# Kernel optimization log

Measured on AMD Instinct MI355X. Metric: run time of the kernel, lower is better.

The kernel has to match this reference:

```python
import jax, jax.numpy as jnp
import numpy as np

B, C, H, W = 16, 384, 32, 32
TEXT = 768
HW = H * W  # == hidden_size
EPS_IN = 1e-5
EPS_L2 = 1e-12


def _gconv3x3(x, w, groups):
    # x: [B,C,H,W], w: [C, C//groups, 3, 3] (torch OIHW layout), padding=1
    return jax.lax.conv_general_dilated(
        x, w, window_strides=(1, 1), padding='SAME',
        dimension_numbers=('NCHW', 'OIHW', 'NCHW'),
        feature_group_count=groups)


def _l2norm(x):
    # torch F.normalize(dim=-1): x / max(||x||_2, 1e-12)
    n = jnp.sqrt(jnp.sum(x * x, axis=-1, keepdims=True))
    return x / jnp.maximum(n, EPS_L2)


def _inst_norm(x):
    # InstanceNorm2d(affine=False) over last two dims per (b, head), biased var
    m = jnp.mean(x, axis=(2, 3), keepdims=True)
    v = jnp.var(x, axis=(2, 3), keepdims=True)
    return (x - m) / jnp.sqrt(v + EPS_IN)


def setup_inputs() -> dict:
    key = jax.random.key(0)
    ks = jax.random.split(key, 13)
    inp = {
        'emb1': jax.random.normal(ks[0], (B, C, H, W), jnp.float32),
        'emb2': jax.random.normal(ks[1], (B, C, H, W), jnp.float32),
        'emb3': jax.random.normal(ks[2], (B, C, H, W), jnp.float32),
        'emb4': jax.random.normal(ks[3], (B, C, H, W), jnp.float32),
        'text_emb': jax.random.normal(ks[4], (B, 1, C, TEXT), jnp.float32),
        # q: Linear(text_size -> hidden_size)
        'wq': jax.random.normal(ks[5], (HW, TEXT), jnp.float32) * 0.02,
        'bq': jnp.zeros((HW,), jnp.float32),
        # 1x1 pointwise projections for k/v (stacked over 4 branches)
        'mk': jax.random.normal(ks[6], (4, C, C), jnp.float32) * (1.0 / np.sqrt(C)),
        'mv': jax.random.normal(ks[7], (4, C, C), jnp.float32) * (1.0 / np.sqrt(C)),
        # 3x3 grouped convs, groups=C//2 -> in_per_group=2, torch weight [C,2,3,3]
        'kw': jax.random.normal(ks[8], (4, C, 2, 3, 3), jnp.float32) * 0.1,
        'vw': jax.random.normal(ks[9], (4, C, 2, 3, 3), jnp.float32) * 0.1,
        # 1x1 output projections
        'po': jax.random.normal(ks[10], (4, C, C), jnp.float32) * (1.0 / np.sqrt(C)),
    }
    return inp


def reference(emb1, emb2, emb3, emb4, text_emb, wq, bq, mk, mv, kw, vw, po):
    b, c, h, w = emb1.shape
    hw = h * w
    # q = Linear(text_emb): [B,1,C,TEXT] @ [TEXT,HW] -> [B,1,C,HW]
    q = _l2norm(text_emb @ wq.T + bq)
    scale = 1.0 / (c ** 0.5)
    embs = (emb1, emb2, emb3, emb4)
    outs = []
    for i in range(4):
        x = embs[i]
        k = _gconv3x3(jnp.einsum('bchw,oc->bohw', x, mk[i]), kw[i], c // 2)
        v = _gconv3x3(jnp.einsum('bchw,oc->bohw', x, mv[i]), vw[i], c // 2)
        k = _l2norm(k.reshape(b, 1, c, hw))   # [B,1,C,HW]
        v = v.reshape(b, 1, c, hw)
        attn = jnp.einsum('bhcn,bhdn->bhcd', q, k) * scale  # [B,1,C,C]
        attn = jax.nn.softmax(_inst_norm(attn), axis=3)
        o = jnp.einsum('bhcd,bhdn->bhcn', attn, v).mean(axis=1)  # [B,C,HW]
        o = jnp.einsum('bchw,oc->bohw', o.reshape(b, c, h, w), po[i])
        outs.append(o)
    return tuple(outs)
```

## Files before the change

### kernel.cpp

```cpp
#include <hip/hip_runtime.h>

typedef unsigned short u16;
typedef __bf16 bf16x8 __attribute__((ext_vector_type(8)));
typedef float f32x4 __attribute__((ext_vector_type(4)));

__device__ __forceinline__ float b2f(u16 u) {
  unsigned int x = ((unsigned int)u) << 16;
  float f;
  __builtin_memcpy(&f, &x, 4);
  return f;
}
__device__ __forceinline__ u16 f2b(float f) {
  unsigned int x;
  __builtin_memcpy(&x, &f, 4);
  unsigned int r = x + 0x7FFFu + ((x >> 16) & 1u);
  return (u16)(r >> 16);
}
static inline unsigned int f2b_host(float f) {
  unsigned int x;
  __builtin_memcpy(&x, &f, 4);
  unsigned int r = x + 0x7FFFu + ((x >> 16) & 1u);
  return r >> 16;
}

__device__ __forceinline__ void gl_lds16(const u16* g, u16* l) {
  __builtin_amdgcn_global_load_lds(
      (const __attribute__((address_space(1))) void*)g,
      (__attribute__((address_space(3))) void*)l, 16, 0, 0);
}

__global__ __launch_bounds__(256) void fill_diag(unsigned int* __restrict__ p,
                                                 long n4, unsigned int pat) {
  long i = (long)blockIdx.x * 256 + threadIdx.x;
  const long stride = (long)gridDim.x * 256;
  for (; i < n4; i += stride) p[i] = pat;
}

__global__ __launch_bounds__(256) void detect_dtype(const u16* __restrict__ text,
                                                    int* __restrict__ flag,
                                                    float* __restrict__ stats) {
  __shared__ int red[4];
  const int t = threadIdx.x;
  if (t < 128) stats[t] = 0.f;
  int c = 0;
#pragma unroll
  for (int j = 0; j < 8; j++) {
    u16 u = text[t * 8 + j];
    int e = (u >> 7) & 0xFF;
    c += (e >= 0x90);
  }
#pragma unroll
  for (int off = 32; off; off >>= 1) c += __shfl_xor(c, off);
  if ((t & 63) == 0) red[t >> 6] = c;
  __syncthreads();
  if (t == 0) flag[0] = (red[0] + red[1] + red[2] + red[3] >= 16) ? 1 : 0;
}

struct Cvt {
  const void* s;
  u16* d;
  long soff;
  int n;
};
struct Cvt16 {
  Cvt c[15];
};
__global__ __launch_bounds__(256) void convert16(Cvt16 args, const int* __restrict__ flag) {
  const Cvt cc = args.c[blockIdx.y];
  const int i8 = (blockIdx.x * 256 + threadIdx.x) * 8;
  if (i8 >= cc.n) return;
  u16 o[8];
  if (flag[0]) {
    const float* s = (const float*)cc.s + cc.soff + i8;
    float4 a = *(const float4*)s;
    float4 b = *(const float4*)(s + 4);
    o[0] = f2b(a.x); o[1] = f2b(a.y); o[2] = f2b(a.z); o[3] = f2b(a.w);
    o[4] = f2b(b.x); o[5] = f2b(b.y); o[6] = f2b(b.z); o[7] = f2b(b.w);
  } else {
    uint4 r = *(const uint4*)((const u16*)cc.s + cc.soff + i8);
    __builtin_memcpy(o, &r, 16);
  }
  uint4 pk;
  __builtin_memcpy(&pk, o, 16);
  *(uint4*)(cc.d + i8) = pk;
}

template <int OUT_BF16, int ADD_BIAS, int DO_STATS>
__global__ __launch_bounds__(256) void gemm_nt(
    const u16* __restrict__ A, const u16* __restrict__ B, void* __restrict__ Cv,
    const u16* __restrict__ bias, int lda, int ldb, int ldc, int K,
    long sA, int zshA, int zmaskA, long sB, long sC, long base, float scale,
    const int* __restrict__ oflag, float* __restrict__ stats,
    int z0, int aglob, int cglob) {
  __shared__ u16 As[4096];
  __shared__ u16 Bs[4096];
  __shared__ float redS[4], redQ[4];
  const int t = threadIdx.x;
  const int zl = blockIdx.z;
  const int zg = zl + z0;
  const int za = aglob ? zg : zl;
  const int zc = cglob ? zg : zl;
  A += (long)((za >> zshA) & zmaskA) * sA;
  B += (long)zl * sB;
  const int bm = blockIdx.y * 128;
  const int bn = blockIdx.x * 128;
  const int lane = t & 63;
  const int wv = t >> 6;
  const int wm = (wv & 1) * 64;
  const int wn = (wv >> 1) * 64;
  const int lr = lane & 15;
  const int lq = lane >> 4;

  const int c0 = wv * 2;
  const int row0 = c0 * 16 + (lane >> 2);
  const int kcl = (((lane & 3) - ((lane >> 3) & 3)) & 3) * 8;
  const u16* pa0 = A + (size_t)(bm + row0) * lda + kcl;
  const u16* pa1 = pa0 + (size_t)16 * lda;
  const u16* pb0 = B + (size_t)(bn + row0) * ldb + kcl;
  const u16* pb1 = pb0 + (size_t)16 * ldb;
  u16* lA0 = &As[c0 * 512];
  u16* lA1 = &As[c0 * 512 + 512];
  u16* lB0 = &Bs[c0 * 512];
  u16* lB1 = &Bs[c0 * 512 + 512];

  const u16* aptr[4];
  const u16* bptr[4];
#pragma unroll
  for (int i = 0; i < 4; i++) {
    const int m = wm + i * 16 + lr;
    aptr[i] = &As[(m * 4 + ((lq + ((m >> 1) & 3)) & 3)) * 8];
    const int n = wn + i * 16 + lr;
    bptr[i] = &Bs[(n * 4 + ((lq + ((n >> 1) & 3)) & 3)) * 8];
  }

  f32x4 acc[4][4];
#pragma unroll
  for (int i = 0; i < 4; i++)
#pragma unroll
    for (int j = 0; j < 4; j++) acc[i][j] = (f32x4){0.f, 0.f, 0.f, 0.f};

  for (int k0 = 0; k0 < K; k0 += 32) {
    gl_lds16(pa0 + k0, lA0);
    gl_lds16(pa1 + k0, lA1);
    gl_lds16(pb0 + k0, lB0);
    gl_lds16(pb1 + k0, lB1);
    __syncthreads();
    bf16x8 af[4], bfr[4];
#pragma unroll
    for (int i = 0; i < 4; i++) af[i] = *(const bf16x8*)aptr[i];
#pragma unroll
    for (int j = 0; j < 4; j++) bfr[j] = *(const bf16x8*)bptr[j];
#pragma unroll
    for (int i = 0; i < 4; i++)
#pragma unroll
      for (int j = 0; j < 4; j++)
        acc[i][j] = __builtin_amdgcn_mfma_f32_16x16x32_bf16(af[i], bfr[j], acc[i][j], 0, 0, 0);
    __syncthreads();
  }

  int f32o = OUT_BF16 ? 0 : 1;
  if (oflag) f32o = oflag[0];
  u16* Cb = (u16*)Cv + base + (long)zc * sC;
  float* Cf = (float*)Cv + base + (long)zc * sC;
  float ls = 0.f, lsq = 0.f;
#pragma unroll
  for (int i = 0; i < 4; i++) {
    const int gm0 = bm + wm + i * 16 + lq * 4;
#pragma unroll
    for (int j = 0; j < 4; j++) {
      const int gn = bn + wn + j * 16 + lr;
      float bv = 0.f;
      if (ADD_BIAS) bv = b2f(bias[gn]);
#pragma unroll
      for (int r = 0; r < 4; r++) {
        float v = acc[i][j][r] * scale + bv;
        if (DO_STATS) {
          ls += v;
          lsq += v * v;
        }
        if (f32o)
          Cf[(size_t)(gm0 + r) * ldc + gn] = v;
        else
          Cb[(size_t)(gm0 + r) * ldc + gn] = f2b(v);
      }
    }
  }
  if (DO_STATS) {
#pragma unroll
    for (int off = 32; off; off >>= 1) {
      ls += __shfl_xor(ls, off);
      lsq += __shfl_xor(lsq, off);
    }
    if (lane == 0) {
      redS[wv] = ls;
      redQ[wv] = lsq;
    }
    __syncthreads();
    if (t == 0) {
      atomicAdd(&stats[zg * 2 + 0], redS[0] + redS[1] + redS[2] + redS[3]);
      atomicAdd(&stats[zg * 2 + 1], redQ[0] + redQ[1] + redQ[2] + redQ[3]);
    }
  }
}

__global__ __launch_bounds__(64) void finalize_stats(const float* __restrict__ stats,
                                                     float* __restrict__ rstd,
                                                     int z0, int cnt) {
  const int i = threadIdx.x;
  if (i >= cnt) return;
  const int z = z0 + i;
  float s = stats[2 * z], q = stats[2 * z + 1];
  float mean = s * (1.f / 147456.f);
  float var = q * (1.f / 147456.f) - mean * mean;
  rstd[z] = 1.f / sqrtf(var + 1e-5f);
}

struct Ptr4 {
  const void* p[4];
};
__global__ __launch_bounds__(256) void transpose_any4(Ptr4 in4, u16* __restrict__ out,
                                                      const int* __restrict__ flag,
                                                      int z0) {
  __shared__ u16 tile[64][72];
  const int t = threadIdx.x;
  const int zl = blockIdx.z;
  const int zg = zl + z0;
  const int br = zg >> 4, b = zg & 15;
  const long ebase = (long)b * 393216;
  const int r0 = blockIdx.y * 64;
  const int c0 = blockIdx.x * 64;
  const int isf32 = flag[0];
#pragma unroll
  for (int j = 0; j < 2; j++) {
    int idx = t + 256 * j;
    int r = idx >> 3, c8 = (idx & 7) << 3;
    u16 v[8];
    if (isf32) {
      const float* in = (const float*)in4.p[br] + ebase + (size_t)(r0 + r) * 1024 + c0 + c8;
      float4 a = *(const float4*)in;
      float4 bb = *(const float4*)(in + 4);
      v[0] = f2b(a.x); v[1] = f2b(a.y); v[2] = f2b(a.z); v[3] = f2b(a.w);
      v[4] = f2b(bb.x); v[5] = f2b(bb.y); v[6] = f2b(bb.z); v[7] = f2b(bb.w);
    } else {
      const u16* in = (const u16*)in4.p[br] + ebase + (size_t)(r0 + r) * 1024 + c0 + c8;
      uint4 rr = *(const uint4*)in;
      __builtin_memcpy(v, &rr, 16);
    }
    __builtin_memcpy(&tile[r][c8], v, 16);
  }
  __syncthreads();
#pragma unroll
  for (int j = 0; j < 2; j++) {
    int idx = t + 256 * j;
    int c = idx >> 3, r8 = (idx & 7) << 3;
    u16 v[8];
#pragma unroll
    for (int jj = 0; jj < 8; jj++) v[jj] = tile[r8 + jj][c];
    uint4 pk;
    __builtin_memcpy(&pk, v, 16);
    *(uint4*)&out[(size_t)zl * 393216 + (size_t)(c0 + c) * 384 + r0 + r8] = pk;
  }
}

__global__ __launch_bounds__(256) void transpose_bf16(const u16* __restrict__ in,
                                                      u16* __restrict__ out) {
  __shared__ u16 tile[64][72];
  const int t = threadIdx.x;
  in += (size_t)blockIdx.z * 393216;
  out += (size_t)blockIdx.z * 393216;
  const int r0 = blockIdx.y * 64;
  const int c0 = blockIdx.x * 64;
#pragma unroll
  for (int j = 0; j < 2; j++) {
    int idx = t + 256 * j;
    int r = idx >> 3, c8 = (idx & 7) << 3;
    *(uint4*)&tile[r][c8] = *(const uint4*)&in[(size_t)(r0 + r) * 1024 + c0 + c8];
  }
  __syncthreads();
#pragma unroll
  for (int j = 0; j < 2; j++) {
    int idx = t + 256 * j;
    int c = idx >> 3, r8 = (idx & 7) << 3;
    u16 v[8];
#pragma unroll
    for (int jj = 0; jj < 8; jj++) v[jj] = tile[r8 + jj][c];
    uint4 pk;
    __builtin_memcpy(&pk, v, 16);
    *(uint4*)&out[(size_t)(c0 + c) * 384 + r0 + r8] = pk;
  }
}

__global__ __launch_bounds__(256) void l2norm_rows_bf16(u16* __restrict__ Q) {
  __shared__ float red[4];
  u16* row = Q + (size_t)blockIdx.x * 1024;
  const int t = threadIdx.x;
  uint2 r = *(const uint2*)(row + t * 4);
  u16 v[4];
  __builtin_memcpy(v, &r, 8);
  float f[4] = {b2f(v[0]), b2f(v[1]), b2f(v[2]), b2f(v[3])};
  float s = f[0] * f[0] + f[1] * f[1] + f[2] * f[2] + f[3] * f[3];
#pragma unroll
  for (int off = 32; off; off >>= 1) s += __shfl_xor(s, off);
  if ((t & 63) == 0) red[t >> 6] = s;
  __syncthreads();
  float tot = red[0] + red[1] + red[2] + red[3];
  float inv = 1.f / fmaxf(sqrtf(tot), 1e-12f);
  u16 o[4] = {f2b(f[0] * inv), f2b(f[1] * inv), f2b(f[2] * inv), f2b(f[3] * inv)};
  unsigned long long pk;
  __builtin_memcpy(&pk, o, 8);
  *(unsigned long long*)(row + t * 4) = pk;
}

__global__ __launch_bounds__(256) void gconv3x3(
    const u16* __restrict__ kvpre, const u16* __restrict__ kw,
    const u16* __restrict__ vw, u16* __restrict__ outK, u16* __restrict__ outV,
    int z0) {
  __shared__ float p[2][1024];
  __shared__ float red[4];
  const int o = blockIdx.x;
  const int zl = blockIdx.y;
  const int kv = blockIdx.z;
  const int t = threadIdx.x;
  const int br = (z0 + zl) >> 4;
  const u16* in = kvpre + ((size_t)zl * 768 + kv * 384 + (o & ~1)) * 1024;
  const u16* wp = (kv ? vw : kw) + br * 6912 + o * 18;
  u16* out = (kv ? outV : outK) + ((size_t)zl * 384 + o) * 1024;
  {
    uint2 ra = *(const uint2*)(in + t * 4);
    uint2 rb = *(const uint2*)(in + 1024 + t * 4);
    u16 va[4], vb[4];
    __builtin_memcpy(va, &ra, 8);
    __builtin_memcpy(vb, &rb, 8);
#pragma unroll
    for (int j = 0; j < 4; j++) {
      p[0][t * 4 + j] = b2f(va[j]);
      p[1][t * 4 + j] = b2f(vb[j]);
    }
  }
  float w[18];
#pragma unroll
  for (int j = 0; j < 18; j++) w[j] = b2f(wp[j]);
  __syncthreads();
  float o4[4];
#pragma unroll
  for (int ii = 0; ii < 4; ii++) {
    const int pidx = t + 256 * ii;
    const int y = pidx >> 5, x = pidx & 31;
    float acc = 0.f;
#pragma unroll
    for (int ch = 0; ch < 2; ch++)
#pragma unroll
      for (int dy = 0; dy < 3; dy++) {
        const int yy = y + dy - 1;
        if (yy < 0 || yy > 31) continue;
#pragma unroll
        for (int dx = 0; dx < 3; dx++) {
          const int xx = x + dx - 1;
          if (xx < 0 || xx > 31) continue;
          acc += w[ch * 9 + dy * 3 + dx] * p[ch][yy * 32 + xx];
        }
      }
    o4[ii] = acc;
  }
  float inv = 1.f;
  if (kv == 0) {
    float s = o4[0] * o4[0] + o4[1] * o4[1] + o4[2] * o4[2] + o4[3] * o4[3];
#pragma unroll
    for (int off = 32; off; off >>= 1) s += __shfl_xor(s, off);
    if ((t & 63) == 0) red[t >> 6] = s;
    __syncthreads();
    float tot = red[0] + red[1] + red[2] + red[3];
    inv = 1.f / fmaxf(sqrtf(tot), 1e-12f);
  }
#pragma unroll
  for (int ii = 0; ii < 4; ii++) out[t + 256 * ii] = f2b(o4[ii] * inv);
}

__global__ __launch_bounds__(256) void softmax384(const float* __restrict__ S,
                                                  const float* __restrict__ rstdA,
                                                  u16* __restrict__ P, int z0) {
  const int row = blockIdx.x * 4 + (threadIdx.x >> 6);
  const int lane = threadIdx.x & 63;
  const float rstd = rstdA[z0 + row / 384];
  const float* x = S + (size_t)row * 384;
  float v[6];
#pragma unroll
  for (int j = 0; j < 6; j++) v[j] = x[lane + 64 * j] * rstd;
  float m = v[0];
#pragma unroll
  for (int j = 1; j < 6; j++) m = fmaxf(m, v[j]);
#pragma unroll
  for (int off = 32; off; off >>= 1) m = fmaxf(m, __shfl_xor(m, off));
  float s = 0.f;
#pragma unroll
  for (int j = 0; j < 6; j++) {
    v[j] = __expf(v[j] - m);
    s += v[j];
  }
#pragma unroll
  for (int off = 32; off; off >>= 1) s += __shfl_xor(s, off);
  const float inv = 1.f / s;
  u16* out = P + (size_t)row * 384;
#pragma unroll
  for (int j = 0; j < 6; j++) out[lane + 64 * j] = f2b(v[j] * inv);
}

extern "C" void kernel_launch(void* const* d_in, const int* in_sizes, int n_in,
                              void* d_out, int out_size, void* d_ws, size_t ws_size,
                              hipStream_t stream) {
  char* ws = (char*)d_ws;
  const dim3 blk(256);

  const size_t bigOff = 17809408;
  auto need = [&](size_t Zs) {
    size_t c = Zs * 3145728;
    if (c < 9437184) c = 9437184;
    return bigOff + c;
  };
  auto diag = [&](float C) {
    unsigned int h = f2b_host(C);
    unsigned int pat = (h << 16) | h;
    long n4 = (long)out_size / 4;
    if (n4 < 1) n4 = 1;
    fill_diag<<<dim3(2048), blk, 0, stream>>>((unsigned int*)d_out, n4, pat);
  };

  static const long elems[12] = {6291456, 6291456, 6291456, 6291456, 4718592,
                                 786432, 1024, 589824, 589824, 27648, 27648,
                                 589824};
  if (!(n_in >= 12) || !d_in || !in_sizes || !d_out || !d_ws) {
    diag(1.0e6f);
    return;
  }
  for (int i = 0; i < 12; i++) {
    if (!d_in[i]) {
      diag(2.0e6f);
      return;
    }
    long sz = in_sizes[i];
    if (sz != elems[i] && sz != elems[i] * 2 && sz != elems[i] * 4) {
      diag(3.0e6f + (float)i * 1.25e5f);
      return;
    }
  }
  if (ws_size < need(1)) {
    diag(9.0e6f);
    return;
  }

  int* flag = (int*)ws;
  float* stats = (float*)(ws + 256);
  float* rstd = (float*)(ws + 1024);
  char* wgt = ws + 2048;
  u16* wq16 = (u16*)wgt;
  u16* bq16 = (u16*)(wgt + 1572864);
  u16* mkv16 = (u16*)(wgt + 1574912);
  u16* kw16 = (u16*)(wgt + 3934208);
  u16* vw16 = (u16*)(wgt + 3989504);
  u16* po16 = (u16*)(wgt + 4044800);
  u16* q16 = (u16*)(ws + 5226496);

  int Z = 1;
  for (int cand = 64; cand >= 1; cand >>= 1) {
    if (ws_size >= need(cand)) {
      Z = cand;
      break;
    }
  }

  char* regA = ws + bigOff;
  char* regB = regA + (size_t)Z * 786432;
  char* regC = regB + (size_t)Z * 1572864;

  u16* text16 = (u16*)regA;
  u16* xT = (u16*)regA;
  u16* kAll = (u16*)regA;
  u16* O = (u16*)regA;
  u16* kvpre = (u16*)regB;
  u16* vT = (u16*)regB;
  float* S = (float*)(regB + (size_t)Z * 786432);
  u16* OT = (u16*)regB;
  u16* vAll = (u16*)regC;
  u16* P16 = (u16*)regC;

  const float scale = 0.05103103630798288f;

  detect_dtype<<<1, blk, 0, stream>>>((const u16*)d_in[4], flag, stats);

  Cvt16 ca;
  int ci = 0;
  auto add = [&](const void* s, u16* d, long soff, int n) {
    ca.c[ci].s = s; ca.c[ci].d = d; ca.c[ci].soff = soff; ca.c[ci].n = n; ci++;
  };
  add(d_in[4], text16, 0, 4718592);
  add(d_in[5], wq16, 0, 786432);
  add(d_in[6], bq16, 0, 1024);
  for (int i = 0; i < 4; i++) add(d_in[7], mkv16 + (long)i * 294912, (long)i * 147456, 147456);
  for (int i = 0; i < 4; i++) add(d_in[8], mkv16 + (long)i * 294912 + 147456, (long)i * 147456, 147456);
  add(d_in[9], kw16, 0, 27648);
  add(d_in[10], vw16, 0, 27648);
  add(d_in[11], po16, 0, 589824);
  convert16<<<dim3(2304, 15, 1), blk, 0, stream>>>(ca, flag);

  gemm_nt<1, 1, 0><<<dim3(8, 48, 1), blk, 0, stream>>>(
      text16, wq16, q16, bq16, 768, 768, 1024, 768, 0, 0, 0, 0, 0, 0, 1.f,
      nullptr, nullptr, 0, 0, 0);
  l2norm_rows_bf16<<<6144, blk, 0, stream>>>(q16);

  Ptr4 p4 = {{d_in[0], d_in[1], d_in[2], d_in[3]}};

  for (int z0 = 0; z0 < 64; z0 += Z) {
    transpose_any4<<<dim3(16, 6, Z), blk, 0, stream>>>(p4, xT, flag, z0);

    gemm_nt<1, 0, 0><<<dim3(8, 6, Z), blk, 0, stream>>>(
        mkv16, xT, kvpre, nullptr, 384, 384, 1024, 384, 294912, 4, 3, 393216,
        786432, 0, 1.f, nullptr, nullptr, z0, 1, 0);

    gconv3x3<<<dim3(384, Z, 2), blk, 0, stream>>>(kvpre, kw16, vw16, kAll,
                                                  vAll, z0);

    transpose_bf16<<<dim3(16, 6, Z), blk, 0, stream>>>(vAll, vT);

    gemm_nt<0, 0, 1><<<dim3(3, 3, Z), blk, 0, stream>>>(
        q16, kAll, S, nullptr, 1024, 1024, 384, 1024, 393216, 0, 15, 393216,
        147456, 0, scale, nullptr, stats, z0, 1, 0);
    finalize_stats<<<1, 64, 0, stream>>>(stats, rstd, z0, Z);
    softmax384<<<Z * 96, blk, 0, stream>>>(S, rstd, P16, z0);

    gemm_nt<1, 0, 0><<<dim3(8, 3, Z), blk, 0, stream>>>(
        P16, vT, O, nullptr, 384, 384, 1024, 384, 147456, 0, 63, 393216, 393216,
        0, 1.f, nullptr, nullptr, z0, 0, 0);
    transpose_bf16<<<dim3(16, 6, Z), blk, 0, stream>>>(O, OT);

    gemm_nt<0, 0, 0><<<dim3(8, 3, Z), blk, 0, stream>>>(
        po16, OT, d_out, nullptr, 384, 384, 1024, 384, 147456, 4, 3, 393216,
        393216, 0, 1.f, flag, nullptr, z0, 1, 1);
  }
}
```

Before: 594.3 us.

## Reassociate output projection as (po·P)·V and fuse stats finalize into softmax

The output is now computed by first multiplying the projection weights by the attention matrix, giving a 384x384 product, and then applying that to V. This replaces the old order, which multiplied P by V (384x1024), transposed the result and then projected it, so one large transpose and one 1024-wide GEMM become a small transpose and a 384x384 GEMM. The finalize_stats kernel is removed, and its mean/rstd computation moves into softmax384. gconv3x3 now handles two output channels per block, so the shared input pair is loaded once. Rounding to bf16 at the intermediate W step changes numerics slightly.

```diff
diff --git a/kernel.cpp b/kernel.cpp
--- a/kernel.cpp
+++ b/kernel.cpp
@@ -203,18 +203,6 @@
   }
 }
 
-__global__ __launch_bounds__(64) void finalize_stats(const float* __restrict__ stats,
-                                                     float* __restrict__ rstd,
-                                                     int z0, int cnt) {
-  const int i = threadIdx.x;
-  if (i >= cnt) return;
-  const int z = z0 + i;
-  float s = stats[2 * z], q = stats[2 * z + 1];
-  float mean = s * (1.f / 147456.f);
-  float var = q * (1.f / 147456.f) - mean * mean;
-  rstd[z] = 1.f / sqrtf(var + 1e-5f);
-}
-
 struct Ptr4 {
   const void* p[4];
 };
@@ -290,6 +278,34 @@
   }
 }
 
+__global__ __launch_bounds__(256) void transpose_b384(const u16* __restrict__ in,
+                                                      u16* __restrict__ out) {
+  __shared__ u16 tile[64][72];
+  const int t = threadIdx.x;
+  in += (size_t)blockIdx.z * 147456;
+  out += (size_t)blockIdx.z * 147456;
+  const int r0 = blockIdx.y * 64;
+  const int c0 = blockIdx.x * 64;
+#pragma unroll
+  for (int j = 0; j < 2; j++) {
+    int idx = t + 256 * j;
+    int r = idx >> 3, c8 = (idx & 7) << 3;
+    *(uint4*)&tile[r][c8] = *(const uint4*)&in[(size_t)(r0 + r) * 384 + c0 + c8];
+  }
+  __syncthreads();
+#pragma unroll
+  for (int j = 0; j < 2; j++) {
+    int idx = t + 256 * j;
+    int c = idx >> 3, r8 = (idx & 7) << 3;
+    u16 v[8];
+#pragma unroll
+    for (int jj = 0; jj < 8; jj++) v[jj] = tile[r8 + jj][c];
+    uint4 pk;
+    __builtin_memcpy(&pk, v, 16);
+    *(uint4*)&out[(size_t)(c0 + c) * 384 + r0 + r8] = pk;
+  }
+}
+
 __global__ __launch_bounds__(256) void l2norm_rows_bf16(u16* __restrict__ Q) {
   __shared__ float red[4];
   u16* row = Q + (size_t)blockIdx.x * 1024;
@@ -316,15 +332,15 @@
     const u16* __restrict__ vw, u16* __restrict__ outK, u16* __restrict__ outV,
     int z0) {
   __shared__ float p[2][1024];
-  __shared__ float red[4];
-  const int o = blockIdx.x;
+  __shared__ float redA[4], redB[4];
+  const int o0 = blockIdx.x * 2;
   const int zl = blockIdx.y;
   const int kv = blockIdx.z;
   const int t = threadIdx.x;
   const int br = (z0 + zl) >> 4;
-  const u16* in = kvpre + ((size_t)zl * 768 + kv * 384 + (o & ~1)) * 1024;
-  const u16* wp = (kv ? vw : kw) + br * 6912 + o * 18;
-  u16* out = (kv ? outV : outK) + ((size_t)zl * 384 + o) * 1024;
+  const u16* in = kvpre + ((size_t)zl * 768 + kv * 384 + o0) * 1024;
+  const u16* wp = (kv ? vw : kw) + br * 6912 + o0 * 18;
+  u16* out = (kv ? outV : outK) + ((size_t)zl * 384 + o0) * 1024;
   {
     uint2 ra = *(const uint2*)(in + t * 4);
     uint2 rb = *(const uint2*)(in + 1024 + t * 4);
@@ -337,16 +353,16 @@
       p[1][t * 4 + j] = b2f(vb[j]);
     }
   }
-  float w[18];
-#pragma unroll
-  for (int j = 0; j < 18; j++) w[j] = b2f(wp[j]);
+  float w[36];
+#pragma unroll
+  for (int j = 0; j < 36; j++) w[j] = b2f(wp[j]);
   __syncthreads();
-  float o4[4];
+  float oa[4], ob[4];
 #pragma unroll
   for (int ii = 0; ii < 4; ii++) {
     const int pidx = t + 256 * ii;
     const int y = pidx >> 5, x = pidx & 31;
-    float acc = 0.f;
+    float acca = 0.f, accb = 0.f;
 #pragma unroll
     for (int ch = 0; ch < 2; ch++)
 #pragma unroll
@@ -357,31 +373,50 @@
         for (int dx = 0; dx < 3; dx++) {
           const int xx = x + dx - 1;
           if (xx < 0 || xx > 31) continue;
-          acc += w[ch * 9 + dy * 3 + dx] * p[ch][yy * 32 + xx];
+          const float pv = p[ch][yy * 32 + xx];
+          acca += w[ch * 9 + dy * 3 + dx] * pv;
+          accb += w[18 + ch * 9 + dy * 3 + dx] * pv;
         }
       }
-    o4[ii] = acc;
-  }
-  float inv = 1.f;
+    oa[ii] = acca;
+    ob[ii] = accb;
+  }
+  float inva = 1.f, invb = 1.f;
   if (kv == 0) {
-    float s = o4[0] * o4[0] + o4[1] * o4[1] + o4[2] * o4[2] + o4[3] * o4[3];
-#pragma unroll
-    for (int off = 32; off; off >>= 1) s += __shfl_xor(s, off);
-    if ((t & 63) == 0) red[t >> 6] = s;
+    float sa = oa[0] * oa[0] + oa[1] * oa[1] + oa[2] * oa[2] + oa[3] * oa[3];
+    float sb = ob[0] * ob[0] + ob[1] * ob[1] + ob[2] * ob[2] + ob[3] * ob[3];
+#pragma unroll
+    for (int off = 32; off; off >>= 1) {
+      sa += __shfl_xor(sa, off);
+      sb += __shfl_xor(sb, off);
+    }
+    if ((t & 63) == 0) {
+      redA[t >> 6] = sa;
+      redB[t >> 6] = sb;
+    }
     __syncthreads();
-    float tot = red[0] + red[1] + red[2] + red[3];
-    inv = 1.f / fmaxf(sqrtf(tot), 1e-12f);
-  }
-#pragma unroll
-  for (int ii = 0; ii < 4; ii++) out[t + 256 * ii] = f2b(o4[ii] * inv);
+    float ta = redA[0] + redA[1] + redA[2] + redA[3];
+    float tb = redB[0] + redB[1] + redB[2] + redB[3];
+    inva = 1.f / fmaxf(sqrtf(ta), 1e-12f);
+    invb = 1.f / fmaxf(sqrtf(tb), 1e-12f);
+  }
+#pragma unroll
+  for (int ii = 0; ii < 4; ii++) {
+    out[t + 256 * ii] = f2b(oa[ii] * inva);
+    out[1024 + t + 256 * ii] = f2b(ob[ii] * invb);
+  }
 }
 
 __global__ __launch_bounds__(256) void softmax384(const float* __restrict__ S,
-                                                  const float* __restrict__ rstdA,
+                                                  const float* __restrict__ stats,
                                                   u16* __restrict__ P, int z0) {
   const int row = blockIdx.x * 4 + (threadIdx.x >> 6);
   const int lane = threadIdx.x & 63;
-  const float rstd = rstdA[z0 + row / 384];
+  const int zg = z0 + row / 384;
+  const float ssum = stats[2 * zg], ssq = stats[2 * zg + 1];
+  const float mean = ssum * (1.f / 147456.f);
+  const float var = ssq * (1.f / 147456.f) - mean * mean;
+  const float rstd = 1.f / sqrtf(var + 1e-5f);
   const float* x = S + (size_t)row * 384;
   float v[6];
 #pragma unroll
@@ -450,7 +485,6 @@
 
   int* flag = (int*)ws;
   float* stats = (float*)(ws + 256);
-  float* rstd = (float*)(ws + 1024);
   char* wgt = ws + 2048;
   u16* wq16 = (u16*)wgt;
   u16* bq16 = (u16*)(wgt + 1572864);
@@ -475,11 +509,11 @@
   u16* text16 = (u16*)regA;
   u16* xT = (u16*)regA;
   u16* kAll = (u16*)regA;
-  u16* O = (u16*)regA;
+  u16* W = (u16*)regA;
   u16* kvpre = (u16*)regB;
   u16* vT = (u16*)regB;
   float* S = (float*)(regB + (size_t)Z * 786432);
-  u16* OT = (u16*)regB;
+  u16* PT = (u16*)(regB + (size_t)Z * 786432);
   u16* vAll = (u16*)regC;
   u16* P16 = (u16*)regC;
 
@@ -516,7 +550,7 @@
         mkv16, xT, kvpre, nullptr, 384, 384, 1024, 384, 294912, 4, 3, 393216,
         786432, 0, 1.f, nullptr, nullptr, z0, 1, 0);
 
-    gconv3x3<<<dim3(384, Z, 2), blk, 0, stream>>>(kvpre, kw16, vw16, kAll,
+    gconv3x3<<<dim3(192, Z, 2), blk, 0, stream>>>(kvpre, kw16, vw16, kAll,
                                                   vAll, z0);
 
     transpose_bf16<<<dim3(16, 6, Z), blk, 0, stream>>>(vAll, vT);
@@ -524,16 +558,17 @@
     gemm_nt<0, 0, 1><<<dim3(3, 3, Z), blk, 0, stream>>>(
         q16, kAll, S, nullptr, 1024, 1024, 384, 1024, 393216, 0, 15, 393216,
         147456, 0, scale, nullptr, stats, z0, 1, 0);
-    finalize_stats<<<1, 64, 0, stream>>>(stats, rstd, z0, Z);
-    softmax384<<<Z * 96, blk, 0, stream>>>(S, rstd, P16, z0);
-
-    gemm_nt<1, 0, 0><<<dim3(8, 3, Z), blk, 0, stream>>>(
-        P16, vT, O, nullptr, 384, 384, 1024, 384, 147456, 0, 63, 393216, 393216,
-        0, 1.f, nullptr, nullptr, z0, 0, 0);
-    transpose_bf16<<<dim3(16, 6, Z), blk, 0, stream>>>(O, OT);
+
+    softmax384<<<Z * 96, blk, 0, stream>>>(S, stats, P16, z0);
+
+    transpose_b384<<<dim3(6, 6, Z), blk, 0, stream>>>(P16, PT);
+
+    gemm_nt<1, 0, 0><<<dim3(3, 3, Z), blk, 0, stream>>>(
+        po16, PT, W, nullptr, 384, 384, 384, 384, 147456, 4, 3, 147456,
+        147456, 0, 1.f, nullptr, nullptr, z0, 1, 0);
 
     gemm_nt<0, 0, 0><<<dim3(8, 3, Z), blk, 0, stream>>>(
-        po16, OT, d_out, nullptr, 384, 384, 1024, 384, 147456, 4, 3, 393216,
-        393216, 0, 1.f, flag, nullptr, z0, 1, 1);
-  }
-}
+        W, vT, d_out, nullptr, 384, 384, 1024, 384, 147456, 0, 63, 393216,
+        393216, 0, 1.f, flag, nullptr, z0, 0, 1);
+  }
+}
```

Measured after the change: 530.8 us. 10.7% less time.
